# Kernel optimization log

Hardware: AMD Instinct MI355X
Metric: run time of the kernel (lower is better)

## Reference

```python
import jax, jax.numpy as jnp
import numpy as np

H, KV, TOPK = 16, 4, 2  # n_head, n_kv_head, n_active_experts
ROPE_BASE = 50000.0

def rmsnorm(x, w):
    return x * jax.lax.rsqrt(jnp.mean(x * x, -1, keepdims=True) + 1e-6) * w

def layernorm_noaffine(x):
    m = jnp.mean(x, -1, keepdims=True)
    v = jnp.var(x, -1, keepdims=True)
    return (x - m) * jax.lax.rsqrt(v + 1e-5)

def rotate_half(x):
    x1, x2 = jnp.split(x, 2, axis=-1)
    return jnp.concatenate([-x2, x1], -1)

def setup_inputs() -> dict:
    key = jax.random.key(0)
    ks = jax.random.split(key, 8)
    B, T, C, F, E = 2, 2048, 1024, 1024, 8
    hd = C // H
    s = 0.02
    return {
        "x": jax.random.normal(ks[0], (B, T, C), jnp.float32),
        "ln1_w": jnp.ones((C,), jnp.float32),
        "ln2_w": jnp.ones((C,), jnp.float32),
        "conv_w": jax.random.normal(ks[1], (C, 3), jnp.float32) * s,
        "c_attn_w": jax.random.normal(ks[2], (C + 2 * KV * hd, C), jnp.float32) * s,
        "c_proj_w": jax.random.normal(ks[3], (C, C), jnp.float32) * s,
        "router_w": jax.random.normal(ks[4], (E, C), jnp.float32) * s,
        "expert_wv": jax.random.normal(ks[5], (E, 2 * F, C), jnp.float32) * s,
        "expert_wo": jax.random.normal(ks[6], (E, C, F), jnp.float32) * s,
    }

def block_forward(x, ln1_w, ln2_w, conv_w, c_attn_w, c_proj_w, router_w, expert_wv, expert_wo):
    B, T, C = x.shape
    hd = C // H
    groups = H // KV
    # --- attention branch ---
    h = rmsnorm(x, ln1_w)
    # causal depthwise conv1d, kernel=3, left pad 2
    xp = jnp.pad(h, ((0, 0), (2, 0), (0, 0)))
    hc = xp[:, 0:T, :] * conv_w[:, 0] + xp[:, 1:T + 1, :] * conv_w[:, 1] + xp[:, 2:T + 2, :] * conv_w[:, 2]
    qkv = hc @ c_attn_w.T
    q = qkv[..., :C].reshape(B, T, H, hd)
    k = qkv[..., C:C + KV * hd].reshape(B, T, KV, hd)
    v = qkv[..., C + KV * hd:].reshape(B, T, KV, hd)
    inv_freq = 1.0 / (ROPE_BASE ** (jnp.arange(0, hd, 2, dtype=jnp.float32) / hd))
    freqs = jnp.arange(T, dtype=jnp.float32)[:, None] * inv_freq[None, :]
    emb = jnp.concatenate([freqs, freqs], -1)
    cos = jnp.cos(emb)[None, :, None, :]  # (1,T,1,hd)
    sin = jnp.sin(emb)[None, :, None, :]
    q = q * cos + rotate_half(q) * sin
    k = k * cos + rotate_half(k) * sin
    k = jnp.repeat(k, groups, axis=2)  # GQA expand
    v = jnp.repeat(v, groups, axis=2)
    q = layernorm_noaffine(q).transpose(0, 2, 1, 3)  # (B,H,T,hd)
    k = layernorm_noaffine(k).transpose(0, 2, 1, 3)
    v = v.transpose(0, 2, 1, 3)
    scores = jnp.einsum('bhqd,bhkd->bhqk', q, k) / jnp.sqrt(jnp.float32(hd))
    mask = jnp.tril(jnp.ones((T, T), bool))
    scores = jnp.where(mask, scores, jnp.finfo(scores.dtype).min)
    att = jax.nn.softmax(scores, -1)
    y = jnp.einsum('bhqk,bhkd->bhqd', att, v).transpose(0, 2, 1, 3).reshape(B, T, C)
    x = x + y @ c_proj_w.T
    # --- MoE branch ---
    h2 = rmsnorm(x, ln2_w)
    logits = h2 @ router_w.T
    probs = jax.nn.softmax(logits, -1)
    weights, indices = jax.lax.top_k(probs, TOPK)
    weights = weights / jnp.sum(weights, -1, keepdims=True)
    E = router_w.shape[0]
    avg = jnp.mean(probs, axis=(0, 1))
    aux_loss = E * jnp.sum(avg * avg)
    N = B * T
    hf = h2.reshape(N, C)
    # dense combine weights (N,E): sum of topk weights scattered to expert slots
    combine = jnp.zeros((N, E), hf.dtype).at[
        jnp.arange(N)[:, None], indices.reshape(N, TOPK)].add(weights.reshape(N, TOPK))
    gv = jnp.einsum('nc,efc->enf', hf, expert_wv)  # (E,N,2F)
    gate, val = jnp.split(gv, 2, axis=-1)
    eh = jax.nn.silu(gate) * val                    # (E,N,F)
    eo = jnp.einsum('enf,ecf->enc', eh, expert_wo)  # (E,N,C)
    moe_out = jnp.einsum('ne,enc->nc', combine, eo).reshape(B, T, C)
    return (x + moe_out, aux_loss)

def reference(x, ln1_w, ln2_w, conv_w, c_attn_w, c_proj_w, router_w, expert_wv, expert_wo):
    return block_forward(x, ln1_w, ln2_w, conv_w, c_attn_w, c_proj_w, router_w, expert_wv, expert_wo)
```

## Files before the change

### kernel.cpp

```cpp
#include <hip/hip_runtime.h>
#include <math.h>

namespace {
constexpr int Bc = 2, Tc = 2048, Cc = 1024, Hc = 16, KVc = 4, HDc = 64, Ec = 8, Fc = 1024;
constexpr int Nc = Bc * Tc;
constexpr int QKVD = Cc + 2 * KVc * HDc;
constexpr int GRP = Hc / KVc;
constexpr float RBASE = 50000.0f;
constexpr int MAXTILES = 72;

constexpr size_t OFF_WQH = 0;
constexpr size_t OFF_WQL = 768u * 1024;
constexpr size_t OFF_WPH = 1536u * 1024;
constexpr size_t OFF_WPL = 2048u * 1024;
constexpr size_t OFF_H   = 2560u * 1024;
constexpr size_t OFF_HCH = 6656u * 1024;
constexpr size_t OFF_HCL = 8704u * 1024;
constexpr size_t OFF_QKV = 10752u * 1024;
constexpr size_t OFF_QHB = 16896u * 1024;
constexpr size_t OFF_QLB = 18944u * 1024;
constexpr size_t OFF_KHB = 20992u * 1024;
constexpr size_t OFF_KLB = 21504u * 1024;
constexpr size_t OFF_VHB = 22016u * 1024;
constexpr size_t OFF_VLB = 22528u * 1024;
constexpr size_t OFF_YH  = 2560u * 1024;
constexpr size_t OFF_YL  = 4608u * 1024;
constexpr size_t OFF_H2   = 0;
constexpr size_t OFF_H2BF = 4u * 1024 * 1024;
constexpr size_t OFF_EHBF = 6u * 1024 * 1024;
constexpr size_t OFF_WVBF = 10u * 1024 * 1024;
constexpr size_t OFF_WOBF = 18u * 1024 * 1024 + 512u * 1024;
constexpr size_t OFF_PROB = 23u * 1024 * 1024;
constexpr size_t OFF_IDX  = OFF_PROB + 32768;
constexpr size_t OFF_WT   = OFF_IDX + 32768;
constexpr size_t OFF_CNT  = OFF_WT + 32768;
constexpr size_t OFF_META = OFF_CNT + 256;
}

typedef __attribute__((ext_vector_type(8))) short short8v;
typedef __attribute__((ext_vector_type(4))) short short4v;
typedef __attribute__((ext_vector_type(4))) float f32x4;

#define MF32(a, b, c) __builtin_amdgcn_mfma_f32_16x16x32_bf16((a), (b), (c), 0, 0, 0)
#define AS1 __attribute__((address_space(1)))
#define AS3 __attribute__((address_space(3)))

__device__ __forceinline__ unsigned short f2b1(float f) {
  union { float f; unsigned int u; } x;
  x.f = f;
  unsigned int r = (x.u + 0x7FFFu + ((x.u >> 16) & 1u)) >> 16;
  return (unsigned short)r;
}

__device__ __forceinline__ float b2f(unsigned short h) {
  union { unsigned int u; float f; } x;
  x.u = (unsigned int)h << 16;
  return x.f;
}

__device__ __forceinline__ void split4(float4 v, short4v& hi, short4v& lo) {
  unsigned short h0 = f2b1(v.x), h1 = f2b1(v.y), h2 = f2b1(v.z), h3 = f2b1(v.w);
  hi = short4v{(short)h0, (short)h1, (short)h2, (short)h3};
  lo = short4v{(short)f2b1(v.x - b2f(h0)), (short)f2b1(v.y - b2f(h1)),
               (short)f2b1(v.z - b2f(h2)), (short)f2b1(v.w - b2f(h3))};
}

__global__ __launch_bounds__(256) void k_rmsnorm(const float* __restrict__ in,
                                                 const float* __restrict__ w,
                                                 float* __restrict__ out) {
  int n = blockIdx.x;
  int tid = threadIdx.x;
  const float* row = in + (size_t)n * Cc;
  float v[4];
  float ss = 0.f;
#pragma unroll
  for (int i = 0; i < 4; i++) {
    v[i] = row[tid + i * 256];
    ss += v[i] * v[i];
  }
#pragma unroll
  for (int m = 1; m < 64; m <<= 1) ss += __shfl_xor(ss, m);
  __shared__ float red[4];
  if ((tid & 63) == 0) red[tid >> 6] = ss;
  __syncthreads();
  float tot = red[0] + red[1] + red[2] + red[3];
  float rs = rsqrtf(tot * (1.0f / Cc) + 1e-6f);
  float* orow = out + (size_t)n * Cc;
#pragma unroll
  for (int i = 0; i < 4; i++) orow[tid + i * 256] = v[i] * rs * w[tid + i * 256];
}

__global__ __launch_bounds__(256) void k_rmsnorm_bf(const float* __restrict__ in,
                                                    const float* __restrict__ w,
                                                    float* __restrict__ out,
                                                    unsigned short* __restrict__ outbf,
                                                    int* __restrict__ cnt) {
  if (blockIdx.x == 0) cnt[threadIdx.x] = 0;
  int n = blockIdx.x;
  int tid = threadIdx.x;
  const float* row = in + (size_t)n * Cc;
  float v[4];
  float ss = 0.f;
#pragma unroll
  for (int i = 0; i < 4; i++) {
    v[i] = row[tid + i * 256];
    ss += v[i] * v[i];
  }
#pragma unroll
  for (int m = 1; m < 64; m <<= 1) ss += __shfl_xor(ss, m);
  __shared__ float red[4];
  if ((tid & 63) == 0) red[tid >> 6] = ss;
  __syncthreads();
  float tot = red[0] + red[1] + red[2] + red[3];
  float rs = rsqrtf(tot * (1.0f / Cc) + 1e-6f);
  float* orow = out + (size_t)n * Cc;
  unsigned short* obf = outbf + (size_t)n * Cc;
#pragma unroll
  for (int i = 0; i < 4; i++) {
    float r = v[i] * rs * w[tid + i * 256];
    orow[tid + i * 256] = r;
    obf[tid + i * 256] = f2b1(r);
  }
}

__global__ __launch_bounds__(256) void k_conv_split(const float* __restrict__ h,
                                                    const float* __restrict__ cw,
                                                    unsigned short* __restrict__ oh,
                                                    unsigned short* __restrict__ ol) {
  int i4 = blockIdx.x * 256 + threadIdx.x;
  if (i4 >= Nc * Cc / 4) return;
  int idx = i4 * 4;
  int c = idx & (Cc - 1);
  int n = idx >> 10;
  int t = n & (Tc - 1);
  float4 z = make_float4(0.f, 0.f, 0.f, 0.f);
  float4 d2 = (t >= 2) ? *(const float4*)&h[idx - 2 * Cc] : z;
  float4 d1 = (t >= 1) ? *(const float4*)&h[idx - Cc] : z;
  float4 d0 = *(const float4*)&h[idx];
  float4 r;
  r.x = d2.x * cw[(c + 0) * 3] + d1.x * cw[(c + 0) * 3 + 1] + d0.x * cw[(c + 0) * 3 + 2];
  r.y = d2.y * cw[(c + 1) * 3] + d1.y * cw[(c + 1) * 3 + 1] + d0.y * cw[(c + 1) * 3 + 2];
  r.z = d2.z * cw[(c + 2) * 3] + d1.z * cw[(c + 2) * 3 + 1] + d0.z * cw[(c + 2) * 3 + 2];
  r.w = d2.w * cw[(c + 3) * 3] + d1.w * cw[(c + 3) * 3 + 1] + d0.w * cw[(c + 3) * 3 + 2];
  short4v hi, lo;
  split4(r, hi, lo);
  *(short4v*)&oh[idx] = hi;
  *(short4v*)&ol[idx] = lo;
}

__global__ __launch_bounds__(256) void k_f2bsp(const float* __restrict__ in,
                                               unsigned short* __restrict__ oh,
                                               unsigned short* __restrict__ ol, int n) {
  int i = (blockIdx.x * 256 + threadIdx.x) * 4;
  if (i >= n) return;
  float4 v = *(const float4*)&in[i];
  short4v hi, lo;
  split4(v, hi, lo);
  *(short4v*)&oh[i] = hi;
  *(short4v*)&ol[i] = lo;
}

__global__ __launch_bounds__(256) void k_f2b(const float* __restrict__ in,
                                             unsigned short* __restrict__ outp, int n) {
  int i = (blockIdx.x * 256 + threadIdx.x) * 4;
  if (i >= n) return;
  float4 v = *(const float4*)&in[i];
  uint2 o;
  o.x = (unsigned int)f2b1(v.x) | ((unsigned int)f2b1(v.y) << 16);
  o.y = (unsigned int)f2b1(v.z) | ((unsigned int)f2b1(v.w) << 16);
  *(uint2*)&outp[i] = o;
}

template <int EPI>
__global__ __launch_bounds__(256) void k_gemm_x3(const unsigned short* __restrict__ Ah,
                                                 const unsigned short* __restrict__ Al,
                                                 const unsigned short* __restrict__ Bh,
                                                 const unsigned short* __restrict__ Bl,
                                                 float* __restrict__ Cm,
                                                 const float* __restrict__ resid,
                                                 int M, int N, int K) {
  constexpr int BM = 128, BN = 64, BK = 32;
  __shared__ __align__(16) unsigned short lAh[BM * BK];
  __shared__ __align__(16) unsigned short lAl[BM * BK];
  __shared__ __align__(16) unsigned short lBh[BN * BK];
  __shared__ __align__(16) unsigned short lBl[BN * BK];
  int tid = threadIdx.x;
  int lane = tid & 63;
  int wave = tid >> 6;
  int wr = wave >> 1, wc = wave & 1;
  int m0 = blockIdx.y * BM, n0 = blockIdx.x * BN;

  f32x4 acc[4][2];
#pragma unroll
  for (int i = 0; i < 4; i++)
#pragma unroll
    for (int j = 0; j < 2; j++) acc[i][j] = (f32x4)0.f;

  int kf = (lane >> 4) * 8;
  int rl = lane & 15;

  const unsigned short* srcA[2];
#pragma unroll
  for (int j = 0; j < 2; j++) {
    int chunk = j * 256 + tid;
    int row = chunk >> 2, cb = (chunk & 3) * 8;
    srcA[j] = (size_t)(m0 + row) * K + cb + Ah;
  }
  int brow = tid >> 2, bcb = (tid & 3) * 8;
  size_t boff = (size_t)(n0 + brow) * K + bcb;

  for (int k0 = 0; k0 < K; k0 += BK) {
    __syncthreads();
#pragma unroll
    for (int j = 0; j < 2; j++) {
      int chunk = j * 256 + tid;
      size_t aoff = (const unsigned short*)srcA[j] - Ah + k0;
      __builtin_amdgcn_global_load_lds((const AS1 void*)(Ah + aoff),
                                       (AS3 void*)(&lAh[chunk * 8]), 16, 0, 0);
      __builtin_amdgcn_global_load_lds((const AS1 void*)(Al + aoff),
                                       (AS3 void*)(&lAl[chunk * 8]), 16, 0, 0);
    }
    __builtin_amdgcn_global_load_lds((const AS1 void*)(Bh + boff + k0),
                                     (AS3 void*)(&lBh[tid * 8]), 16, 0, 0);
    __builtin_amdgcn_global_load_lds((const AS1 void*)(Bl + boff + k0),
                                     (AS3 void*)(&lBl[tid * 8]), 16, 0, 0);
    asm volatile("s_waitcnt vmcnt(0)" ::: "memory");
    __syncthreads();

    short8v ah[4], al4[4], bh4[2], bl4[2];
#pragma unroll
    for (int i = 0; i < 4; i++) {
      int ro = (wr * 64 + i * 16 + rl) * BK + kf;
      ah[i] = *(const short8v*)&lAh[ro];
      al4[i] = *(const short8v*)&lAl[ro];
    }
#pragma unroll
    for (int j = 0; j < 2; j++) {
      int ro = (wc * 32 + j * 16 + rl) * BK + kf;
      bh4[j] = *(const short8v*)&lBh[ro];
      bl4[j] = *(const short8v*)&lBl[ro];
    }
#pragma unroll
    for (int i = 0; i < 4; i++)
#pragma unroll
      for (int j = 0; j < 2; j++) {
        acc[i][j] = MF32(ah[i], bh4[j], acc[i][j]);
        acc[i][j] = MF32(ah[i], bl4[j], acc[i][j]);
        acc[i][j] = MF32(al4[i], bh4[j], acc[i][j]);
      }
  }

  int cl = lane & 15;
  int rb = (lane >> 4) * 4;
#pragma unroll
  for (int i = 0; i < 4; i++) {
#pragma unroll
    for (int r = 0; r < 4; r++) {
      int m = m0 + wr * 64 + i * 16 + rb + r;
#pragma unroll
      for (int j = 0; j < 2; j++) {
        int n = n0 + wc * 32 + j * 16 + cl;
        size_t off = (size_t)m * N + n;
        if (EPI == 0) Cm[off] = acc[i][j][r];
        else Cm[off] = resid[off] + acc[i][j][r];
      }
    }
  }
}

__global__ __launch_bounds__(256) void k_moe_wv(const unsigned short* __restrict__ A,
                                                const unsigned short* __restrict__ Wv,
                                                unsigned short* __restrict__ Eh,
                                                const int* __restrict__ idx,
                                                const int* __restrict__ cnt,
                                                const int* __restrict__ meta) {
  constexpr int BK = 32;
  if ((int)blockIdx.y >= meta[16 + 8]) return;
  int e = 0;
#pragma unroll
  for (int i = 1; i < Ec; i++)
    if ((int)blockIdx.y >= meta[16 + i]) e = i;
  int lm = blockIdx.y - meta[16 + e];
  int count = cnt[e * 32];
  int gb = meta[e];
  int m0 = lm * 128;
  int n0 = blockIdx.x * 64;

  __shared__ __align__(16) unsigned short lA[128 * BK];
  __shared__ __align__(16) unsigned short lBg[64 * BK];
  __shared__ __align__(16) unsigned short lBv[64 * BK];
  int tid = threadIdx.x;
  int lane = tid & 63;
  int wave = tid >> 6;
  int wr = wave >> 1, wc = wave & 1;

  const unsigned short* srcA[2];
  const unsigned short* srcG;
  const unsigned short* srcV;
#pragma unroll
  for (int j = 0; j < 2; j++) {
    int chunk = j * 256 + tid;
    int row = chunk >> 2, cb = (chunk & 3) * 8;
    int mrow = m0 + row;
    int tok = idx[e * Nc + (mrow < count ? mrow : count - 1)];
    srcA[j] = A + (size_t)tok * Cc + cb;
  }
  {
    int row = tid >> 2, cb = (tid & 3) * 8;
    const unsigned short* wbase = Wv + (size_t)e * 2 * Fc * Cc;
    srcG = wbase + (size_t)(n0 + row) * Cc + cb;
    srcV = wbase + (size_t)(Fc + n0 + row) * Cc + cb;
  }

  f32x4 accG[4][2], accV[4][2];
#pragma unroll
  for (int i = 0; i < 4; i++)
#pragma unroll
    for (int j = 0; j < 2; j++) {
      accG[i][j] = (f32x4)0.f;
      accV[i][j] = (f32x4)0.f;
    }

  int kf = (lane >> 4) * 8;
  int rl = lane & 15;

  for (int k0 = 0; k0 < Cc; k0 += BK) {
    __syncthreads();
#pragma unroll
    for (int j = 0; j < 2; j++) {
      int chunk = j * 256 + tid;
      __builtin_amdgcn_global_load_lds((const AS1 void*)(srcA[j] + k0),
                                       (AS3 void*)(&lA[chunk * 8]), 16, 0, 0);
    }
    __builtin_amdgcn_global_load_lds((const AS1 void*)(srcG + k0),
                                     (AS3 void*)(&lBg[tid * 8]), 16, 0, 0);
    __builtin_amdgcn_global_load_lds((const AS1 void*)(srcV + k0),
                                     (AS3 void*)(&lBv[tid * 8]), 16, 0, 0);
    asm volatile("s_waitcnt vmcnt(0)" ::: "memory");
    __syncthreads();

    short8v a[4], bg[2], bv[2];
#pragma unroll
    for (int i = 0; i < 4; i++)
      a[i] = *(const short8v*)&lA[(wr * 64 + i * 16 + rl) * BK + kf];
#pragma unroll
    for (int j = 0; j < 2; j++) {
      bg[j] = *(const short8v*)&lBg[(wc * 32 + j * 16 + rl) * BK + kf];
      bv[j] = *(const short8v*)&lBv[(wc * 32 + j * 16 + rl) * BK + kf];
    }
#pragma unroll
    for (int i = 0; i < 4; i++)
#pragma unroll
      for (int j = 0; j < 2; j++) {
        accG[i][j] = MF32(a[i], bg[j], accG[i][j]);
        accV[i][j] = MF32(a[i], bv[j], accV[i][j]);
      }
  }

  int cl = lane & 15;
  int rb = (lane >> 4) * 4;
#pragma unroll
  for (int i = 0; i < 4; i++) {
#pragma unroll
    for (int r = 0; r < 4; r++) {
      int m = m0 + wr * 64 + i * 16 + rb + r;
      if (m < count) {
        size_t gs = (size_t)(gb + m);
#pragma unroll
        for (int j = 0; j < 2; j++) {
          int n = n0 + wc * 32 + j * 16 + cl;
          float g = accG[i][j][r];
          float v = accV[i][j][r];
          Eh[gs * Fc + n] = f2b1(g / (1.0f + __expf(-g)) * v);
        }
      }
    }
  }
}

__global__ __launch_bounds__(256) void k_moe_wo(const unsigned short* __restrict__ Eh,
                                                const unsigned short* __restrict__ Wo,
                                                float* __restrict__ C,
                                                const int* __restrict__ idx,
                                                const float* __restrict__ wt,
                                                const int* __restrict__ cnt,
                                                const int* __restrict__ meta) {
  constexpr int BK = 32;
  if ((int)blockIdx.y >= meta[16 + 8]) return;
  int e = 0;
#pragma unroll
  for (int i = 1; i < Ec; i++)
    if ((int)blockIdx.y >= meta[16 + i]) e = i;
  int lm = blockIdx.y - meta[16 + e];
  int count = cnt[e * 32];
  int gb = meta[e];
  int m0 = lm * 128;
  int n0 = blockIdx.x * 128;

  __shared__ __align__(16) unsigned short lA[128 * BK];
  __shared__ __align__(16) unsigned short lB[128 * BK];
  int tid = threadIdx.x;
  int lane = tid & 63;
  int wave = tid >> 6;
  int wr = wave >> 1, wc = wave & 1;

  f32x4 acc[4][4];
#pragma unroll
  for (int i = 0; i < 4; i++)
#pragma unroll
    for (int j = 0; j < 4; j++) acc[i][j] = (f32x4)0.f;

  int kf = (lane >> 4) * 8;
  int rl = lane & 15;

  for (int k0 = 0; k0 < Fc; k0 += BK) {
    __syncthreads();
#pragma unroll
    for (int j = 0; j < 2; j++) {
      int chunk = j * 256 + tid;
      int row = chunk >> 2;
      int cb = (chunk & 3) * 8;
      __builtin_amdgcn_global_load_lds(
          (const AS1 void*)(Eh + (size_t)(gb + m0 + row) * Fc + k0 + cb),
          (AS3 void*)(&lA[chunk * 8]), 16, 0, 0);
      __builtin_amdgcn_global_load_lds(
          (const AS1 void*)(Wo + (size_t)e * Cc * Fc + (size_t)(n0 + row) * Fc + k0 + cb),
          (AS3 void*)(&lB[chunk * 8]), 16, 0, 0);
    }
    asm volatile("s_waitcnt vmcnt(0)" ::: "memory");
    __syncthreads();

    short8v a[4], b[4];
#pragma unroll
    for (int i = 0; i < 4; i++)
      a[i] = *(const short8v*)&lA[(wr * 64 + i * 16 + rl) * BK + kf];
#pragma unroll
    for (int j = 0; j < 4; j++)
      b[j] = *(const short8v*)&lB[(wc * 64 + j * 16 + rl) * BK + kf];
#pragma unroll
    for (int i = 0; i < 4; i++)
#pragma unroll
      for (int j = 0; j < 4; j++)
        acc[i][j] = MF32(a[i], b[j], acc[i][j]);
  }

  int cl = lane & 15;
  int rb = (lane >> 4) * 4;
#pragma unroll
  for (int i = 0; i < 4; i++) {
#pragma unroll
    for (int r = 0; r < 4; r++) {
      int m = m0 + wr * 64 + i * 16 + rb + r;
      if (m < count) {
        int slot = e * Nc + m;
        int tok = idx[slot];
        float w = wt[slot];
#pragma unroll
        for (int j = 0; j < 4; j++) {
          int n = n0 + wc * 64 + j * 16 + cl;
          atomicAdd(&C[(size_t)tok * Cc + n], w * acc[i][j][r]);
        }
      }
    }
  }
}

__device__ __forceinline__ float rope_ln(float q, int lane, int t, float scale) {
  int j = lane & 31;
  float invf = powf(RBASE, -(float)j * (1.0f / 32.0f));
  float ang = (float)t * invf;
  float s, c;
  sincosf(ang, &s, &c);
  float p = __shfl_xor(q, 32);
  float rot = (lane < 32) ? -p : p;
  float qr = q * c + rot * s;
  float sum = qr, sq = qr * qr;
#pragma unroll
  for (int m = 1; m < 64; m <<= 1) {
    sum += __shfl_xor(sum, m);
    sq += __shfl_xor(sq, m);
  }
  float mean = sum * (1.0f / 64.0f);
  float var = sq * (1.0f / 64.0f) - mean * mean;
  return (qr - mean) * rsqrtf(var + 1e-5f) * scale;
}

__global__ __launch_bounds__(256) void k_ropeln_q(const float* __restrict__ qkv,
                                                  unsigned short* __restrict__ qh,
                                                  unsigned short* __restrict__ ql) {
  int gw = (blockIdx.x * 256 + threadIdx.x) >> 6;
  int lane = threadIdx.x & 63;
  if (gw >= Nc * Hc) return;
  int h = gw & (Hc - 1);
  int n = gw / Hc;
  int t = n & (Tc - 1);
  int b = n / Tc;
  float q = qkv[(size_t)n * QKVD + h * HDc + lane];
  float o = rope_ln(q, lane, t, 0.125f);
  int row = t & 63;
  size_t ob = (((size_t)(b * Hc + h)) * 32 + (t >> 6)) * 4096 + row * 64 +
              (lane ^ ((row & 7) << 3));
  unsigned short hi = f2b1(o);
  qh[ob] = hi;
  ql[ob] = f2b1(o - b2f(hi));
}

__global__ __launch_bounds__(256) void k_ropeln_kv(const float* __restrict__ qkv,
                                                   unsigned short* __restrict__ kh,
                                                   unsigned short* __restrict__ kl,
                                                   unsigned short* __restrict__ vh,
                                                   unsigned short* __restrict__ vl) {
  int gw = (blockIdx.x * 256 + threadIdx.x) >> 6;
  int lane = threadIdx.x & 63;
  if (gw >= Nc * KVc) return;
  int kv = gw & (KVc - 1);
  int n = gw / KVc;
  int t = n & (Tc - 1);
  int b = n / Tc;
  size_t base = (size_t)n * QKVD + Cc + kv * HDc;
  float kval = qkv[base + lane];
  float vval = qkv[base + KVc * HDc + lane];
  float o = rope_ln(kval, lane, t, 1.0f);
  int row = t & 63;
  size_t tb = (((size_t)(b * KVc + kv)) * 32 + (t >> 6)) * 4096;
  size_t ko = tb + row * 64 + (lane ^ ((row & 7) << 3));
  unsigned short khi = f2b1(o);
  kh[ko] = khi;
  kl[ko] = f2b1(o - b2f(khi));
  size_t vo = tb + (size_t)lane * 64 + (row ^ ((lane & 7) << 3));
  unsigned short vhi = f2b1(vval);
  vh[vo] = vhi;
  vl[vo] = f2b1(vval - b2f(vhi));
}

__global__ __launch_bounds__(256, 3) void k_attn2(const unsigned short* __restrict__ Qh,
                                                  const unsigned short* __restrict__ Ql,
                                                  const unsigned short* __restrict__ Kht,
                                                  const unsigned short* __restrict__ Klt,
                                                  const unsigned short* __restrict__ Vht,
                                                  const unsigned short* __restrict__ Vlt,
                                                  unsigned short* __restrict__ Yh,
                                                  unsigned short* __restrict__ Yl) {
  __shared__ __align__(16) unsigned char smem[49152];
  constexpr unsigned QH = 0, QL = 8192, KH = 16384, KL = 24576, VB = 32768, PB = 0;
  int tid = threadIdx.x;
  int l = tid & 63, w = tid >> 6, g = l >> 4, q15 = l & 15;
  int bx = blockIdx.x;
  int hh = blockIdx.y, b = blockIdx.z;
  int kvh = hh >> 2;
  size_t kvb = ((size_t)(b * KVc + kvh)) * 32 * 4096;
  unsigned qsw = (unsigned)((q15 & 7) << 4);
  unsigned qro = (unsigned)((w * 16 + q15) * 128);
  int qloc = w * 16 + q15;

  for (int which = 0; which < 2; ++which) {
    int qtile = which == 0 ? (Tc / 64 - 1 - bx) : bx;
    size_t qtb = (((size_t)(b * Hc + hh)) * 32 + qtile) * 4096;
    __syncthreads();
#pragma unroll
    for (int j = 0; j < 2; j++) {
      int chunk = j * 256 + tid;
      __builtin_amdgcn_global_load_lds((const AS1 void*)(Qh + qtb + chunk * 8),
                                       (AS3 void*)(smem + QH + chunk * 16), 16, 0, 0);
      __builtin_amdgcn_global_load_lds((const AS1 void*)(Ql + qtb + chunk * 8),
                                       (AS3 void*)(smem + QL + chunk * 16), 16, 0, 0);
    }
    asm volatile("s_waitcnt vmcnt(0)" ::: "memory");
    __syncthreads();
    short8v qhf[2], qlf[2];
    qhf[0] = *(const short8v*)(smem + QH + qro + ((16 * g) ^ qsw));
    qhf[1] = *(const short8v*)(smem + QH + qro + ((64 + 16 * g) ^ qsw));
    qlf[0] = *(const short8v*)(smem + QL + qro + ((16 * g) ^ qsw));
    qlf[1] = *(const short8v*)(smem + QL + qro + ((64 + 16 * g) ^ qsw));

    f32x4 o[4];
#pragma unroll
    for (int dt = 0; dt < 4; dt++) o[dt] = (f32x4)0.f;
    float m = -1e30f, lsum = 0.f;

    for (int kt = 0; kt <= qtile; ++kt) {
      __syncthreads();
      size_t ktb = kvb + (size_t)kt * 4096;
#pragma unroll
      for (int j = 0; j < 2; j++) {
        int chunk = j * 256 + tid;
        __builtin_amdgcn_global_load_lds((const AS1 void*)(Kht + ktb + chunk * 8),
                                         (AS3 void*)(smem + KH + chunk * 16), 16, 0, 0);
        __builtin_amdgcn_global_load_lds((const AS1 void*)(Klt + ktb + chunk * 8),
                                         (AS3 void*)(smem + KL + chunk * 16), 16, 0, 0);
        __builtin_amdgcn_global_load_lds((const AS1 void*)(Vht + ktb + chunk * 8),
                                         (AS3 void*)(smem + VB + chunk * 16), 16, 0, 0);
        __builtin_amdgcn_global_load_lds((const AS1 void*)(Vlt + ktb + chunk * 8),
                                         (AS3 void*)(smem + VB + 8192 + chunk * 16), 16, 0,
                                         0);
      }
      asm volatile("s_waitcnt vmcnt(0)" ::: "memory");
      __syncthreads();
      const bool diag = (kt == qtile);

      f32x4 sv[4];
#pragma unroll
      for (int s = 0; s < 4; ++s) {
        unsigned ro = (unsigned)((s * 16 + q15) * 128);
        short8v kh0 = *(const short8v*)(smem + KH + ro + ((16 * g) ^ qsw));
        short8v kh1 = *(const short8v*)(smem + KH + ro + ((64 + 16 * g) ^ qsw));
        short8v kl0 = *(const short8v*)(smem + KL + ro + ((16 * g) ^ qsw));
        short8v kl1 = *(const short8v*)(smem + KL + ro + ((64 + 16 * g) ^ qsw));
        f32x4 a = (f32x4)0.f;
        a = MF32(kh0, qhf[0], a);
        a = MF32(kh1, qhf[1], a);
        a = MF32(kh0, qlf[0], a);
        a = MF32(kh1, qlf[1], a);
        a = MF32(kl0, qhf[0], a);
        a = MF32(kl1, qhf[1], a);
        sv[s] = a;
      }
      float mx = -1e30f;
#pragma unroll
      for (int s = 0; s < 4; ++s)
#pragma unroll
        for (int r = 0; r < 4; ++r) {
          if (diag && (s * 16 + g * 4 + r) > qloc) sv[s][r] = -1e30f;
          mx = fmaxf(mx, sv[s][r]);
        }
      mx = fmaxf(mx, __shfl_xor(mx, 16));
      mx = fmaxf(mx, __shfl_xor(mx, 32));
      float mnew = fmaxf(m, mx);
      float alpha = __expf(m - mnew);
      float p[4][4];
      float ps = 0.f;
#pragma unroll
      for (int s = 0; s < 4; ++s)
#pragma unroll
        for (int r = 0; r < 4; ++r) {
          p[s][r] = __expf(sv[s][r] - mnew);
          ps += p[s][r];
        }
      ps += __shfl_xor(ps, 16);
      ps += __shfl_xor(ps, 32);
      lsum = lsum * alpha + ps;
      m = mnew;
#pragma unroll
      for (int dt = 0; dt < 4; dt++) o[dt] *= alpha;
#pragma unroll
      for (int s = 0; s < 4; ++s) {
        unsigned short h0 = f2b1(p[s][0]), h1 = f2b1(p[s][1]), h2 = f2b1(p[s][2]),
                       h3 = f2b1(p[s][3]);
        short4v ph = short4v{(short)h0, (short)h1, (short)h2, (short)h3};
        short4v pl = short4v{(short)f2b1(p[s][0] - b2f(h0)), (short)f2b1(p[s][1] - b2f(h1)),
                             (short)f2b1(p[s][2] - b2f(h2)), (short)f2b1(p[s][3] - b2f(h3))};
        unsigned pb = (unsigned)(PB + w * 4096 + q15 * 128 +
                                 (((unsigned)(s * 32 + 8 * g)) ^ qsw));
        *(short4v*)(smem + pb) = ph;
        *(short4v*)(smem + pb + 2048) = pl;
      }
      asm volatile("" ::: "memory");
#pragma unroll
      for (int kk = 0; kk < 2; ++kk) {
        unsigned pq = (unsigned)(PB + w * 4096 + q15 * 128 +
                                 (((unsigned)(kk * 64 + 16 * g)) ^ qsw));
        short8v ph8 = *(const short8v*)(smem + pq);
        short8v pl8 = *(const short8v*)(smem + pq + 2048);
        unsigned koff = (unsigned)(kk * 64 + g * 16);
#pragma unroll
        for (int dt = 0; dt < 4; ++dt) {
          unsigned off = VB + (unsigned)((dt * 16 + q15) * 128) + (koff ^ qsw);
          short8v vh8 = *(const short8v*)(smem + off);
          short8v vl8 = *(const short8v*)(smem + off + 8192);
          o[dt] = MF32(vh8, ph8, o[dt]);
          o[dt] = MF32(vh8, pl8, o[dt]);
          o[dt] = MF32(vl8, ph8, o[dt]);
        }
      }
    }
    float inv = 1.0f / lsum;
    size_t ybase = ((size_t)(b * Tc + qtile * 64 + qloc)) * Cc + hh * 64;
#pragma unroll
    for (int dt = 0; dt < 4; dt++) {
      float4 s4 = make_float4(o[dt][0] * inv, o[dt][1] * inv, o[dt][2] * inv,
                              o[dt][3] * inv);
      short4v hi, lo;
      split4(s4, hi, lo);
      *(short4v*)&Yh[ybase + dt * 16 + 4 * g] = hi;
      *(short4v*)&Yl[ybase + dt * 16 + 4 * g] = lo;
    }
  }
}

__global__ void k_meta(const int* __restrict__ cnt, int* __restrict__ meta) {
  if (threadIdx.x == 0) {
    int gb = 0, tb = 0;
    for (int e = 0; e < Ec; e++) {
      meta[e] = gb;
      meta[16 + e] = tb;
      gb += cnt[e * 32];
      tb += (cnt[e * 32] + 127) >> 7;
    }
    meta[8] = gb;
    meta[16 + 8] = tb;
  }
}

__global__ __launch_bounds__(256) void k_router(const float* __restrict__ h2,
                                                const float* __restrict__ rw,
                                                float* __restrict__ probs,
                                                int* __restrict__ idx,
                                                float* __restrict__ wt,
                                                int* __restrict__ cnt) {
  int gw = (blockIdx.x * 256 + threadIdx.x) >> 6;
  int lane = threadIdx.x & 63;
  if (gw >= Nc) return;
  const float* row = h2 + (size_t)gw * Cc;
  float acc[Ec] = {};
  for (int k = lane; k < Cc; k += 64) {
    float hv = row[k];
#pragma unroll
    for (int e = 0; e < Ec; e++) acc[e] += hv * rw[e * Cc + k];
  }
#pragma unroll
  for (int e = 0; e < Ec; e++) {
#pragma unroll
    for (int msk = 1; msk < 64; msk <<= 1) acc[e] += __shfl_xor(acc[e], msk);
  }
  if (lane == 0) {
    float mx = acc[0];
#pragma unroll
    for (int e = 1; e < Ec; e++) mx = fmaxf(mx, acc[e]);
    float p[Ec];
    float s = 0.f;
#pragma unroll
    for (int e = 0; e < Ec; e++) {
      p[e] = expf(acc[e] - mx);
      s += p[e];
    }
    float invs = 1.0f / s;
#pragma unroll
    for (int e = 0; e < Ec; e++) {
      p[e] *= invs;
      probs[(size_t)gw * Ec + e] = p[e];
    }
    int i0 = 0;
#pragma unroll
    for (int e = 1; e < Ec; e++)
      if (p[e] > p[i0]) i0 = e;
    int i1 = (i0 == 0) ? 1 : 0;
#pragma unroll
    for (int e = 0; e < Ec; e++)
      if (e != i0 && p[e] > p[i1]) i1 = e;
    float wsum = p[i0] + p[i1];
    int s0 = atomicAdd(&cnt[i0 * 32], 1);
    int s1 = atomicAdd(&cnt[i1 * 32], 1);
    idx[i0 * Nc + s0] = gw;
    wt[i0 * Nc + s0] = p[i0] / wsum;
    idx[i1 * Nc + s1] = gw;
    wt[i1 * Nc + s1] = p[i1] / wsum;
  }
}

__global__ __launch_bounds__(256) void k_aux(const float* __restrict__ probs,
                                             float* __restrict__ outp) {
  int tid = threadIdx.x;
  int lane = tid & 63, w = tid >> 6;
  float acc[Ec] = {};
  for (int n = tid; n < Nc; n += 256) {
#pragma unroll
    for (int e = 0; e < Ec; e++) acc[e] += probs[(size_t)n * Ec + e];
  }
#pragma unroll
  for (int e = 0; e < Ec; e++) {
#pragma unroll
    for (int msk = 1; msk < 64; msk <<= 1) acc[e] += __shfl_xor(acc[e], msk);
  }
  __shared__ float red[4][Ec];
  if (lane == 0) {
#pragma unroll
    for (int e = 0; e < Ec; e++) red[w][e] = acc[e];
  }
  __syncthreads();
  if (tid == 0) {
    float aux = 0.f;
#pragma unroll
    for (int e = 0; e < Ec; e++) {
      float tot = red[0][e] + red[1][e] + red[2][e] + red[3][e];
      float avg = tot * (1.0f / Nc);
      aux += avg * avg;
    }
    outp[0] = (float)Ec * aux;
  }
}

extern "C" void kernel_launch(void* const* d_in, const int* in_sizes, int n_in,
                              void* d_out, int out_size, void* d_ws, size_t ws_size,
                              hipStream_t stream) {
  const float* x      = (const float*)d_in[0];
  const float* ln1_w  = (const float*)d_in[1];
  const float* ln2_w  = (const float*)d_in[2];
  const float* conv_w = (const float*)d_in[3];
  const float* attn_w = (const float*)d_in[4];
  const float* proj_w = (const float*)d_in[5];
  const float* rout_w = (const float*)d_in[6];
  const float* ewv    = (const float*)d_in[7];
  const float* ewo    = (const float*)d_in[8];
  float* out = (float*)d_out;
  float* ws = (float*)d_ws;

  float* h    = ws + OFF_H;
  float* qkv  = ws + OFF_QKV;
  float* h2   = ws + OFF_H2;
  float* prob = ws + OFF_PROB;
  int*   idxp = (int*)(ws + OFF_IDX);
  float* wtp  = ws + OFF_WT;
  int*   cntp = (int*)(ws + OFF_CNT);
  int*   metap = (int*)(ws + OFF_META);
  unsigned short* wqh = (unsigned short*)(ws + OFF_WQH);
  unsigned short* wql = (unsigned short*)(ws + OFF_WQL);
  unsigned short* wph = (unsigned short*)(ws + OFF_WPH);
  unsigned short* wpl = (unsigned short*)(ws + OFF_WPL);
  unsigned short* hch = (unsigned short*)(ws + OFF_HCH);
  unsigned short* hcl = (unsigned short*)(ws + OFF_HCL);
  unsigned short* qhb = (unsigned short*)(ws + OFF_QHB);
  unsigned short* qlb = (unsigned short*)(ws + OFF_QLB);
  unsigned short* khb = (unsigned short*)(ws + OFF_KHB);
  unsigned short* klb = (unsigned short*)(ws + OFF_KLB);
  unsigned short* vhb = (unsigned short*)(ws + OFF_VHB);
  unsigned short* vlb = (unsigned short*)(ws + OFF_VLB);
  unsigned short* yh  = (unsigned short*)(ws + OFF_YH);
  unsigned short* yl  = (unsigned short*)(ws + OFF_YL);
  unsigned short* h2bf = (unsigned short*)(ws + OFF_H2BF);
  unsigned short* ehbf = (unsigned short*)(ws + OFF_EHBF);
  unsigned short* wvbf = (unsigned short*)(ws + OFF_WVBF);
  unsigned short* wobf = (unsigned short*)(ws + OFF_WOBF);

  k_rmsnorm<<<Nc, 256, 0, stream>>>(x, ln1_w, h);
  k_conv_split<<<(Nc * Cc / 4) / 256, 256, 0, stream>>>(h, conv_w, hch, hcl);
  k_f2bsp<<<(QKVD * Cc / 4) / 256, 256, 0, stream>>>(attn_w, wqh, wql, QKVD * Cc);
  k_f2bsp<<<(Cc * Cc / 4) / 256, 256, 0, stream>>>(proj_w, wph, wpl, Cc * Cc);
  {
    dim3 g(QKVD / 64, Nc / 128);
    k_gemm_x3<0><<<g, 256, 0, stream>>>(hch, hcl, wqh, wql, qkv, nullptr, Nc, QKVD, Cc);
  }
  k_ropeln_q<<<(Nc * Hc * 64) / 256, 256, 0, stream>>>(qkv, qhb, qlb);
  k_ropeln_kv<<<(Nc * KVc * 64) / 256, 256, 0, stream>>>(qkv, khb, klb, vhb, vlb);
  k_attn2<<<dim3(Tc / 128, Hc, Bc), 256, 0, stream>>>(qhb, qlb, khb, klb, vhb, vlb, yh, yl);
  {
    dim3 g(Cc / 64, Nc / 128);
    k_gemm_x3<1><<<g, 256, 0, stream>>>(yh, yl, wph, wpl, out, x, Nc, Cc, Cc);
  }
  k_rmsnorm_bf<<<Nc, 256, 0, stream>>>(out, ln2_w, h2, h2bf, cntp);
  k_router<<<Nc / 4, 256, 0, stream>>>(h2, rout_w, prob, idxp, wtp, cntp);
  k_meta<<<1, 64, 0, stream>>>(cntp, metap);
  k_aux<<<1, 256, 0, stream>>>(prob, out + (size_t)Nc * Cc);
  k_f2b<<<(Ec * 2 * Fc * Cc / 4) / 256, 256, 0, stream>>>(ewv, wvbf, Ec * 2 * Fc * Cc);
  k_f2b<<<(Ec * Cc * Fc / 4) / 256, 256, 0, stream>>>(ewo, wobf, Ec * Cc * Fc);
  k_moe_wv<<<dim3(Fc / 64, MAXTILES), 256, 0, stream>>>(h2bf, wvbf, ehbf, idxp, cntp, metap);
  k_moe_wo<<<dim3(Cc / 128, MAXTILES), 256, 0, stream>>>(ehbf, wobf, out, idxp, wtp, cntp,
                                                         metap);
}
```

Baseline: 428.7 us.

## Share K/V tile loads between paired causal query tiles in attention

The attention kernel used to process its two paired query tiles (a late one and an early one) one after the other, streaming K/V tiles from global memory for each. Now both query tiles' fragments stay in registers and one K/V loop serves both. The early tile's step runs only while kt <= qtB, which cuts global-to-LDS traffic and barriers for the shorter tile. The cost is higher register pressure from a second accumulator set and a second copy of the Q fragments, which may lower occupancy.

After: 431.6 us. No clear change (+0.7%).

```diff
diff --git a/kernel.cpp b/kernel.cpp
--- a/kernel.cpp
+++ b/kernel.cpp
@@ -552,11 +552,12 @@
   unsigned qsw = (unsigned)((q15 & 7) << 4);
   unsigned qro = (unsigned)((w * 16 + q15) * 128);
   int qloc = w * 16 + q15;
-
-  for (int which = 0; which < 2; ++which) {
-    int qtile = which == 0 ? (Tc / 64 - 1 - bx) : bx;
-    size_t qtb = (((size_t)(b * Hc + hh)) * 32 + qtile) * 4096;
-    __syncthreads();
+  int qtA = Tc / 64 - 1 - bx;
+  int qtB = bx;
+
+  short8v qahf[2], qalf[2], qbhf[2], qblf[2];
+  {
+    size_t qtb = (((size_t)(b * Hc + hh)) * 32 + qtA) * 4096;
 #pragma unroll
     for (int j = 0; j < 2; j++) {
       int chunk = j * 256 + tid;
@@ -567,123 +568,158 @@
     }
     asm volatile("s_waitcnt vmcnt(0)" ::: "memory");
     __syncthreads();
-    short8v qhf[2], qlf[2];
-    qhf[0] = *(const short8v*)(smem + QH + qro + ((16 * g) ^ qsw));
-    qhf[1] = *(const short8v*)(smem + QH + qro + ((64 + 16 * g) ^ qsw));
-    qlf[0] = *(const short8v*)(smem + QL + qro + ((16 * g) ^ qsw));
-    qlf[1] = *(const short8v*)(smem + QL + qro + ((64 + 16 * g) ^ qsw));
-
-    f32x4 o[4];
-#pragma unroll
-    for (int dt = 0; dt < 4; dt++) o[dt] = (f32x4)0.f;
-    float m = -1e30f, lsum = 0.f;
-
-    for (int kt = 0; kt <= qtile; ++kt) {
-      __syncthreads();
-      size_t ktb = kvb + (size_t)kt * 4096;
-#pragma unroll
-      for (int j = 0; j < 2; j++) {
-        int chunk = j * 256 + tid;
-        __builtin_amdgcn_global_load_lds((const AS1 void*)(Kht + ktb + chunk * 8),
-                                         (AS3 void*)(smem + KH + chunk * 16), 16, 0, 0);
-        __builtin_amdgcn_global_load_lds((const AS1 void*)(Klt + ktb + chunk * 8),
-                                         (AS3 void*)(smem + KL + chunk * 16), 16, 0, 0);
-        __builtin_amdgcn_global_load_lds((const AS1 void*)(Vht + ktb + chunk * 8),
-                                         (AS3 void*)(smem + VB + chunk * 16), 16, 0, 0);
-        __builtin_amdgcn_global_load_lds((const AS1 void*)(Vlt + ktb + chunk * 8),
-                                         (AS3 void*)(smem + VB + 8192 + chunk * 16), 16, 0,
-                                         0);
+    qahf[0] = *(const short8v*)(smem + QH + qro + ((16 * g) ^ qsw));
+    qahf[1] = *(const short8v*)(smem + QH + qro + ((64 + 16 * g) ^ qsw));
+    qalf[0] = *(const short8v*)(smem + QL + qro + ((16 * g) ^ qsw));
+    qalf[1] = *(const short8v*)(smem + QL + qro + ((64 + 16 * g) ^ qsw));
+    __syncthreads();
+    size_t qtb2 = (((size_t)(b * Hc + hh)) * 32 + qtB) * 4096;
+#pragma unroll
+    for (int j = 0; j < 2; j++) {
+      int chunk = j * 256 + tid;
+      __builtin_amdgcn_global_load_lds((const AS1 void*)(Qh + qtb2 + chunk * 8),
+                                       (AS3 void*)(smem + QH + chunk * 16), 16, 0, 0);
+      __builtin_amdgcn_global_load_lds((const AS1 void*)(Ql + qtb2 + chunk * 8),
+                                       (AS3 void*)(smem + QL + chunk * 16), 16, 0, 0);
+    }
+    asm volatile("s_waitcnt vmcnt(0)" ::: "memory");
+    __syncthreads();
+    qbhf[0] = *(const short8v*)(smem + QH + qro + ((16 * g) ^ qsw));
+    qbhf[1] = *(const short8v*)(smem + QH + qro + ((64 + 16 * g) ^ qsw));
+    qblf[0] = *(const short8v*)(smem + QL + qro + ((16 * g) ^ qsw));
+    qblf[1] = *(const short8v*)(smem + QL + qro + ((64 + 16 * g) ^ qsw));
+  }
+
+  f32x4 oA[4], oB[4];
+#pragma unroll
+  for (int dt = 0; dt < 4; dt++) {
+    oA[dt] = (f32x4)0.f;
+    oB[dt] = (f32x4)0.f;
+  }
+  float mA = -1e30f, lsA = 0.f, mB = -1e30f, lsB = 0.f;
+
+  auto STEP = [&](const short8v* qhf, const short8v* qlf, f32x4* o, float& m,
+                  float& lsum, bool diag) {
+    f32x4 sv[4];
+#pragma unroll
+    for (int s = 0; s < 4; ++s) {
+      unsigned ro = (unsigned)((s * 16 + q15) * 128);
+      short8v kh0 = *(const short8v*)(smem + KH + ro + ((16 * g) ^ qsw));
+      short8v kh1 = *(const short8v*)(smem + KH + ro + ((64 + 16 * g) ^ qsw));
+      short8v kl0 = *(const short8v*)(smem + KL + ro + ((16 * g) ^ qsw));
+      short8v kl1 = *(const short8v*)(smem + KL + ro + ((64 + 16 * g) ^ qsw));
+      f32x4 a = (f32x4)0.f;
+      a = MF32(kh0, qhf[0], a);
+      a = MF32(kh1, qhf[1], a);
+      a = MF32(kh0, qlf[0], a);
+      a = MF32(kh1, qlf[1], a);
+      a = MF32(kl0, qhf[0], a);
+      a = MF32(kl1, qhf[1], a);
+      sv[s] = a;
+    }
+    float mx = -1e30f;
+#pragma unroll
+    for (int s = 0; s < 4; ++s)
+#pragma unroll
+      for (int r = 0; r < 4; ++r) {
+        if (diag && (s * 16 + g * 4 + r) > qloc) sv[s][r] = -1e30f;
+        mx = fmaxf(mx, sv[s][r]);
       }
-      asm volatile("s_waitcnt vmcnt(0)" ::: "memory");
-      __syncthreads();
-      const bool diag = (kt == qtile);
-
-      f32x4 sv[4];
-#pragma unroll
-      for (int s = 0; s < 4; ++s) {
-        unsigned ro = (unsigned)((s * 16 + q15) * 128);
-        short8v kh0 = *(const short8v*)(smem + KH + ro + ((16 * g) ^ qsw));
-        short8v kh1 = *(const short8v*)(smem + KH + ro + ((64 + 16 * g) ^ qsw));
-        short8v kl0 = *(const short8v*)(smem + KL + ro + ((16 * g) ^ qsw));
-        short8v kl1 = *(const short8v*)(smem + KL + ro + ((64 + 16 * g) ^ qsw));
-        f32x4 a = (f32x4)0.f;
-        a = MF32(kh0, qhf[0], a);
-        a = MF32(kh1, qhf[1], a);
-        a = MF32(kh0, qlf[0], a);
-        a = MF32(kh1, qlf[1], a);
-        a = MF32(kl0, qhf[0], a);
-        a = MF32(kl1, qhf[1], a);
-        sv[s] = a;
+    mx = fmaxf(mx, __shfl_xor(mx, 16));
+    mx = fmaxf(mx, __shfl_xor(mx, 32));
+    float mnew = fmaxf(m, mx);
+    float alpha = __expf(m - mnew);
+    float p[4][4];
+    float ps = 0.f;
+#pragma unroll
+    for (int s = 0; s < 4; ++s)
+#pragma unroll
+      for (int r = 0; r < 4; ++r) {
+        p[s][r] = __expf(sv[s][r] - mnew);
+        ps += p[s][r];
       }
-      float mx = -1e30f;
-#pragma unroll
-      for (int s = 0; s < 4; ++s)
-#pragma unroll
-        for (int r = 0; r < 4; ++r) {
-          if (diag && (s * 16 + g * 4 + r) > qloc) sv[s][r] = -1e30f;
-          mx = fmaxf(mx, sv[s][r]);
-        }
-      mx = fmaxf(mx, __shfl_xor(mx, 16));
-      mx = fmaxf(mx, __shfl_xor(mx, 32));
-      float mnew = fmaxf(m, mx);
-      float alpha = __expf(m - mnew);
-      float p[4][4];
-      float ps = 0.f;
-#pragma unroll
-      for (int s = 0; s < 4; ++s)
-#pragma unroll
-        for (int r = 0; r < 4; ++r) {
-          p[s][r] = __expf(sv[s][r] - mnew);
-          ps += p[s][r];
-        }
-      ps += __shfl_xor(ps, 16);
-      ps += __shfl_xor(ps, 32);
-      lsum = lsum * alpha + ps;
-      m = mnew;
-#pragma unroll
-      for (int dt = 0; dt < 4; dt++) o[dt] *= alpha;
-#pragma unroll
-      for (int s = 0; s < 4; ++s) {
-        unsigned short h0 = f2b1(p[s][0]), h1 = f2b1(p[s][1]), h2 = f2b1(p[s][2]),
-                       h3 = f2b1(p[s][3]);
-        short4v ph = short4v{(short)h0, (short)h1, (short)h2, (short)h3};
-        short4v pl = short4v{(short)f2b1(p[s][0] - b2f(h0)), (short)f2b1(p[s][1] - b2f(h1)),
-                             (short)f2b1(p[s][2] - b2f(h2)), (short)f2b1(p[s][3] - b2f(h3))};
-        unsigned pb = (unsigned)(PB + w * 4096 + q15 * 128 +
-                                 (((unsigned)(s * 32 + 8 * g)) ^ qsw));
-        *(short4v*)(smem + pb) = ph;
-        *(short4v*)(smem + pb + 2048) = pl;
+    ps += __shfl_xor(ps, 16);
+    ps += __shfl_xor(ps, 32);
+    lsum = lsum * alpha + ps;
+    m = mnew;
+#pragma unroll
+    for (int dt = 0; dt < 4; dt++) o[dt] *= alpha;
+#pragma unroll
+    for (int s = 0; s < 4; ++s) {
+      unsigned short h0 = f2b1(p[s][0]), h1 = f2b1(p[s][1]), h2 = f2b1(p[s][2]),
+                     h3 = f2b1(p[s][3]);
+      short4v ph = short4v{(short)h0, (short)h1, (short)h2, (short)h3};
+      short4v pl = short4v{(short)f2b1(p[s][0] - b2f(h0)), (short)f2b1(p[s][1] - b2f(h1)),
+                           (short)f2b1(p[s][2] - b2f(h2)), (short)f2b1(p[s][3] - b2f(h3))};
+      unsigned pb = (unsigned)(PB + w * 4096 + q15 * 128 +
+                               (((unsigned)(s * 32 + 8 * g)) ^ qsw));
+      *(short4v*)(smem + pb) = ph;
+      *(short4v*)(smem + pb + 2048) = pl;
+    }
+    asm volatile("" ::: "memory");
+#pragma unroll
+    for (int kk = 0; kk < 2; ++kk) {
+      unsigned pq = (unsigned)(PB + w * 4096 + q15 * 128 +
+                               (((unsigned)(kk * 64 + 16 * g)) ^ qsw));
+      short8v ph8 = *(const short8v*)(smem + pq);
+      short8v pl8 = *(const short8v*)(smem + pq + 2048);
+      unsigned koff = (unsigned)(kk * 64 + g * 16);
+#pragma unroll
+      for (int dt = 0; dt < 4; ++dt) {
+        unsigned off = VB + (unsigned)((dt * 16 + q15) * 128) + (koff ^ qsw);
+        short8v vh8 = *(const short8v*)(smem + off);
+        short8v vl8 = *(const short8v*)(smem + off + 8192);
+        o[dt] = MF32(vh8, ph8, o[dt]);
+        o[dt] = MF32(vh8, pl8, o[dt]);
+        o[dt] = MF32(vl8, ph8, o[dt]);
       }
-      asm volatile("" ::: "memory");
-#pragma unroll
-      for (int kk = 0; kk < 2; ++kk) {
-        unsigned pq = (unsigned)(PB + w * 4096 + q15 * 128 +
-                                 (((unsigned)(kk * 64 + 16 * g)) ^ qsw));
-        short8v ph8 = *(const short8v*)(smem + pq);
-        short8v pl8 = *(const short8v*)(smem + pq + 2048);
-        unsigned koff = (unsigned)(kk * 64 + g * 16);
-#pragma unroll
-        for (int dt = 0; dt < 4; ++dt) {
-          unsigned off = VB + (unsigned)((dt * 16 + q15) * 128) + (koff ^ qsw);
-          short8v vh8 = *(const short8v*)(smem + off);
-          short8v vl8 = *(const short8v*)(smem + off + 8192);
-          o[dt] = MF32(vh8, ph8, o[dt]);
-          o[dt] = MF32(vh8, pl8, o[dt]);
-          o[dt] = MF32(vl8, ph8, o[dt]);
-        }
-      }
-    }
-    float inv = 1.0f / lsum;
-    size_t ybase = ((size_t)(b * Tc + qtile * 64 + qloc)) * Cc + hh * 64;
-#pragma unroll
-    for (int dt = 0; dt < 4; dt++) {
-      float4 s4 = make_float4(o[dt][0] * inv, o[dt][1] * inv, o[dt][2] * inv,
-                              o[dt][3] * inv);
-      short4v hi, lo;
-      split4(s4, hi, lo);
-      *(short4v*)&Yh[ybase + dt * 16 + 4 * g] = hi;
-      *(short4v*)&Yl[ybase + dt * 16 + 4 * g] = lo;
-    }
+    }
+  };
+
+  for (int kt = 0; kt <= qtA; ++kt) {
+    __syncthreads();
+    size_t ktb = kvb + (size_t)kt * 4096;
+#pragma unroll
+    for (int j = 0; j < 2; j++) {
+      int chunk = j * 256 + tid;
+      __builtin_amdgcn_global_load_lds((const AS1 void*)(Kht + ktb + chunk * 8),
+                                       (AS3 void*)(smem + KH + chunk * 16), 16, 0, 0);
+      __builtin_amdgcn_global_load_lds((const AS1 void*)(Klt + ktb + chunk * 8),
+                                       (AS3 void*)(smem + KL + chunk * 16), 16, 0, 0);
+      __builtin_amdgcn_global_load_lds((const AS1 void*)(Vht + ktb + chunk * 8),
+                                       (AS3 void*)(smem + VB + chunk * 16), 16, 0, 0);
+      __builtin_amdgcn_global_load_lds((const AS1 void*)(Vlt + ktb + chunk * 8),
+                                       (AS3 void*)(smem + VB + 8192 + chunk * 16), 16, 0,
+                                       0);
+    }
+    asm volatile("s_waitcnt vmcnt(0)" ::: "memory");
+    __syncthreads();
+
+    STEP(qahf, qalf, oA, mA, lsA, kt == qtA);
+    if (kt <= qtB) STEP(qbhf, qblf, oB, mB, lsB, kt == qtB);
+  }
+
+  float invA = 1.0f / lsA;
+  size_t ybA = ((size_t)(b * Tc + qtA * 64 + qloc)) * Cc + hh * 64;
+#pragma unroll
+  for (int dt = 0; dt < 4; dt++) {
+    float4 s4 = make_float4(oA[dt][0] * invA, oA[dt][1] * invA, oA[dt][2] * invA,
+                            oA[dt][3] * invA);
+    short4v hi, lo;
+    split4(s4, hi, lo);
+    *(short4v*)&Yh[ybA + dt * 16 + 4 * g] = hi;
+    *(short4v*)&Yl[ybA + dt * 16 + 4 * g] = lo;
+  }
+  float invB = 1.0f / lsB;
+  size_t ybB = ((size_t)(b * Tc + qtB * 64 + qloc)) * Cc + hh * 64;
+#pragma unroll
+  for (int dt = 0; dt < 4; dt++) {
+    float4 s4 = make_float4(oB[dt][0] * invB, oB[dt][1] * invB, oB[dt][2] * invB,
+                            oB[dt][3] * invB);
+    short4v hi, lo;
+    split4(s4, hi, lo);
+    *(short4v*)&Yh[ybB + dt * 16 + 4 * g] = hi;
+    *(short4v*)&Yl[ybB + dt * 16 + 4 * g] = lo;
   }
 }
 
```
